# Kernel optimization log

Hardware: AMD Instinct MI355X
Metric: run time of the kernel (lower is better)

Reference implementation:

```python
import jax, jax.numpy as jnp
import numpy as np

B, E, T = 16, 64, 1000
DIM, HEADS, NB_F, LAYERS, NUM_CLASSES = 32, 4, 64, 2, 2
BAND_K = 51
DH = DIM // HEADS  # head dim = 8
EPS = 1e-5


def _layernorm(x, g, b):
    mu = jnp.mean(x, axis=-1, keepdims=True)
    var = jnp.var(x, axis=-1, keepdims=True)
    return (x - mu) * jax.lax.rsqrt(var + EPS) * g + b


def setup_inputs() -> dict:
    key = jax.random.key(0)
    ks = jax.random.split(key, 24)
    d = {}
    d['x'] = jax.random.normal(ks[0], (B, 1, E, T), dtype=jnp.float32)
    # fixed band-pass filters, stacked as one conv: [4 out, 1 in, 1, 51]
    d['band_w'] = jax.random.normal(ks[1], (4, 1, 1, BAND_K), dtype=jnp.float32) * 0.1
    d['pw_w'] = jax.random.normal(ks[2], (DIM, 4), dtype=jnp.float32) * 0.5
    d['bn_g'] = jnp.ones((DIM,), jnp.float32)
    d['bn_b'] = jnp.zeros((DIM,), jnp.float32)
    d['bn_m'] = jnp.zeros((DIM,), jnp.float32)
    d['bn_v'] = jnp.ones((DIM,), jnp.float32)
    s = 1.0 / np.sqrt(DIM)
    L = LAYERS
    d['ln1_g'] = jnp.ones((L, DIM), jnp.float32)
    d['ln1_b'] = jnp.zeros((L, DIM), jnp.float32)
    d['wqkv'] = jax.random.normal(ks[3], (L, DIM, 3 * DIM), jnp.float32) * s
    d['proj_mat'] = jax.random.normal(ks[4], (L, HEADS, DH, NB_F), jnp.float32)
    d['wproj'] = jax.random.normal(ks[5], (L, DIM, DIM), jnp.float32) * s
    d['bproj'] = jnp.zeros((L, DIM), jnp.float32)
    d['ln2_g'] = jnp.ones((L, DIM), jnp.float32)
    d['ln2_b'] = jnp.zeros((L, DIM), jnp.float32)
    d['w1'] = jax.random.normal(ks[6], (L, DIM, 2 * DIM), jnp.float32) * s
    d['b1'] = jnp.zeros((L, 2 * DIM), jnp.float32)
    d['w2'] = jax.random.normal(ks[7], (L, 2 * DIM, DIM), jnp.float32) * (1.0 / np.sqrt(2 * DIM))
    d['b2'] = jnp.zeros((L, DIM), jnp.float32)
    d['norm_g'] = jnp.ones((DIM,), jnp.float32)
    d['norm_b'] = jnp.zeros((DIM,), jnp.float32)
    d['pool_w'] = jax.random.normal(ks[8], (DIM, 1), jnp.float32) * s
    d['pool_b'] = jnp.zeros((1,), jnp.float32)
    d['fc_w'] = jax.random.normal(ks[9], (DIM, NUM_CLASSES), jnp.float32) * s
    d['fc_b'] = jnp.zeros((NUM_CLASSES,), jnp.float32)
    return d


def _favor(x, pm):
    # x: [B,N,C] -> [B,N,H,F] feature map
    b, n, c = x.shape
    xh = x.reshape(b, n, HEADS, DH)
    p = jnp.einsum('bnhd,hdf->bnhf', xh, pm)
    return jax.nn.elu(p) + 1.0


def _attn(x, wqkv, pm, wproj, bproj):
    b, n, c = x.shape
    qkv = x @ wqkv  # [B,N,3C]
    q, k, v = jnp.split(qkv, 3, axis=-1)
    Q = _favor(q, pm)
    K = _favor(k, pm)
    V = v.reshape(b, n, HEADS, DH)
    # NOTE: faithful to source — KV sums over batch AND sequence
    KV = jnp.einsum('bnhf,bnhd->hfd', K, V)
    Z = 1.0 / jnp.einsum('bnhf,hfd->bnh', Q, KV)
    out = jnp.einsum('bnhf,hfd->bnhd', Q, KV) * Z[..., None]
    return out.reshape(b, n, c) @ wproj + bproj


def _tokenize(x, band_w, pw_w, bn_g, bn_b, bn_m, bn_v):
    pad = BAND_K // 2
    xc = jax.lax.conv_general_dilated(
        x, band_w, window_strides=(1, 1), padding=((0, 0), (pad, pad)),
        dimension_numbers=('NCHW', 'OIHW', 'NCHW'))  # [B,4,E,T]
    h = jnp.einsum('bcet,oc->boet', xc, pw_w)  # 1x1 conv -> [B,DIM,E,T]
    h = (h - bn_m[:, None, None]) * jax.lax.rsqrt(bn_v[:, None, None] + EPS) \
        * bn_g[:, None, None] + bn_b[:, None, None]
    h = jax.nn.gelu(h, approximate=False)
    b, c, e, t = h.shape
    h = h.reshape(b, c, e, t // 4, 4).mean(axis=-1)  # AvgPool (1,4)
    h = h.reshape(b, c, e * (t // 4))
    return jnp.transpose(h, (0, 2, 1))  # [B, N, DIM]


def reference(x, band_w, pw_w, bn_g, bn_b, bn_m, bn_v, ln1_g, ln1_b, wqkv,
              proj_mat, wproj, bproj, ln2_g, ln2_b, w1, b1, w2, b2,
              norm_g, norm_b, pool_w, pool_b, fc_w, fc_b):
    h = _tokenize(x, band_w, pw_w, bn_g, bn_b, bn_m, bn_v)
    for l in range(LAYERS):
        h = h + _attn(_layernorm(h, ln1_g[l], ln1_b[l]), wqkv[l], proj_mat[l],
                      wproj[l], bproj[l])
        m = _layernorm(h, ln2_g[l], ln2_b[l])
        m = jax.nn.gelu(m @ w1[l] + b1[l], approximate=False) @ w2[l] + b2[l]
        h = h + m
    h = _layernorm(h, norm_g, norm_b)
    w = jax.nn.softmax(h @ pool_w + pool_b, axis=1)  # [B,N,1]
    pooled = jnp.sum(w * h, axis=1)  # [B,DIM]
    return pooled @ fc_w + fc_b
```

## Files before the change

### kernel.cpp

```cpp
#include <hip/hip_runtime.h>
#include <math.h>

#define NTOK   256000
#define TOKB   16000
#define EPS    1e-5f

__device__ __forceinline__ float gelu_f(float x){
  return 0.5f*x*(1.0f+erff(x*0.70710678118654752440f));
}
__device__ __forceinline__ float elu1_f(float x){
  return x>0.0f ? x+1.0f : __expf(x);
}

__global__ __launch_bounds__(256) void k_tokenize(
    const float* __restrict__ x, const float* __restrict__ band_w,
    const float* __restrict__ pw_w, const float* __restrict__ bn_g,
    const float* __restrict__ bn_b, const float* __restrict__ bn_m,
    const float* __restrict__ bn_v, float* __restrict__ hout)
{
  __shared__ float sx[1050];
  __shared__ float sbw[4][51];
  __shared__ float spw[32][4];
  __shared__ float sscale[32], sshift[32];
  const int tid = threadIdx.x;
  const int b = blockIdx.x >> 6, e = blockIdx.x & 63;
  const float* xr = x + (size_t)(b*64 + e)*1000;
  for (int i=tid;i<1050;i+=256){ int t=i-25; sx[i]=(t>=0&&t<1000)?xr[t]:0.0f; }
  for (int i=tid;i<204;i+=256){ sbw[i/51][i%51] = band_w[i]; }
  for (int i=tid;i<128;i+=256){ spw[i>>2][i&3] = pw_w[i]; }
  if (tid<32){ float sc = bn_g[tid]*rsqrtf(bn_v[tid]+EPS);
               sscale[tid]=sc; sshift[tid]=bn_b[tid]-bn_m[tid]*sc; }
  __syncthreads();
  const int tp = tid;
  if (tp < 250) {
    float acc[32];
    #pragma unroll
    for (int o=0;o<32;o++) acc[o]=0.0f;
    for (int j=0;j<4;j++){
      const int t = 4*tp+j;
      float c0=0,c1=0,c2=0,c3=0;
      for (int k=0;k<51;k++){
        float xv = sx[t+k];
        c0 += xv*sbw[0][k]; c1 += xv*sbw[1][k];
        c2 += xv*sbw[2][k]; c3 += xv*sbw[3][k];
      }
      #pragma unroll
      for (int o=0;o<32;o++){
        float hv = spw[o][0]*c0 + spw[o][1]*c1 + spw[o][2]*c2 + spw[o][3]*c3;
        hv = hv*sscale[o] + sshift[o];
        acc[o] += gelu_f(hv);
      }
    }
    const int tok = b*TOKB + e*250 + tp;
    float4* dst = (float4*)(hout + (size_t)tok*32);
    #pragma unroll
    for (int o8=0;o8<8;o8++)
      dst[o8] = make_float4(acc[o8*4]*0.25f, acc[o8*4+1]*0.25f,
                            acc[o8*4+2]*0.25f, acc[o8*4+3]*0.25f);
  }
}

__global__ __launch_bounds__(256) void k_kv_partial(
    const float* __restrict__ hbuf, const float* __restrict__ ln1_g,
    const float* __restrict__ ln1_b, const float* __restrict__ wqkv,
    const float* __restrict__ proj_mat, float* __restrict__ kvpart, int l)
{
  __shared__ __align__(16) float sk[128][36];
  __shared__ __align__(16) float sv[128][36];
  __shared__ __align__(16) float swkT[64][32];
  __shared__ float sg[32], sb[32];
  const int tid = threadIdx.x;
  const float* W = wqkv + l*32*96;
  for (int idx=tid;idx<2048;idx+=256){
    int i = idx&31, j = idx>>5;
    swkT[j][i] = W[i*96 + 32 + j];
  }
  if (tid<32){ sg[tid]=ln1_g[l*32+tid]; sb[tid]=ln1_b[l*32+tid]; }
  __syncthreads();
  {
    const int tloc = tid>>1, half = tid&1;
    const int tok = blockIdx.x*128 + tloc;
    float hx[32];
    const float4* src = (const float4*)(hbuf + (size_t)tok*32);
    #pragma unroll
    for (int i=0;i<8;i++){ float4 v4=src[i]; hx[4*i]=v4.x; hx[4*i+1]=v4.y; hx[4*i+2]=v4.z; hx[4*i+3]=v4.w; }
    float mu=0;
    #pragma unroll
    for (int i=0;i<32;i++) mu += hx[i];
    mu *= (1.0f/32.0f);
    float vs=0;
    #pragma unroll
    for (int i=0;i<32;i++){ float d=hx[i]-mu; vs += d*d; }
    const float inv = rsqrtf(vs*(1.0f/32.0f)+EPS);
    float xn[32];
    #pragma unroll
    for (int i=0;i<32;i++) xn[i] = (hx[i]-mu)*inv*sg[i]+sb[i];
    const int j0 = half*16;
    #pragma unroll 4
    for (int jj=0;jj<16;jj++){
      const int j = j0+jj;
      const float4* wk4 = (const float4*)&swkT[j][0];
      const float4* wv4 = (const float4*)&swkT[32+j][0];
      float ka=0, va=0;
      #pragma unroll
      for (int i4=0;i4<8;i4++){
        float4 wk = wk4[i4], wv = wv4[i4];
        ka += xn[4*i4+0]*wk.x + xn[4*i4+1]*wk.y + xn[4*i4+2]*wk.z + xn[4*i4+3]*wk.w;
        va += xn[4*i4+0]*wv.x + xn[4*i4+1]*wv.y + xn[4*i4+2]*wv.z + xn[4*i4+3]*wv.w;
      }
      sk[tloc][j]=ka; sv[tloc][j]=va;
    }
  }
  __syncthreads();
  const int hh = tid>>6, f = tid&63;
  float pm0,pm1,pm2,pm3,pm4,pm5,pm6,pm7;
  {
    const float* pmp = proj_mat + ((size_t)(l*4+hh)*8)*64 + f;
    pm0=pmp[0]; pm1=pmp[64]; pm2=pmp[128]; pm3=pmp[192];
    pm4=pmp[256]; pm5=pmp[320]; pm6=pmp[384]; pm7=pmp[448];
  }
  float a0=0,a1=0,a2=0,a3=0,a4=0,a5=0,a6=0,a7=0;
  #pragma unroll 4
  for (int t=0;t<128;t++){
    const float4* k4 = (const float4*)&sk[t][hh*8];
    const float4* v4 = (const float4*)&sv[t][hh*8];
    float4 ka = k4[0], kb = k4[1];
    float kd = ka.x*pm0 + ka.y*pm1 + ka.z*pm2 + ka.w*pm3
             + kb.x*pm4 + kb.y*pm5 + kb.z*pm6 + kb.w*pm7;
    const float Kf = elu1_f(kd);
    float4 va = v4[0], vb = v4[1];
    a0 += Kf*va.x; a1 += Kf*va.y; a2 += Kf*va.z; a3 += Kf*va.w;
    a4 += Kf*vb.x; a5 += Kf*vb.y; a6 += Kf*vb.z; a7 += Kf*vb.w;
  }
  float4* dst = (float4*)(kvpart + (size_t)blockIdx.x*2048 + tid*8);
  dst[0] = make_float4(a0,a1,a2,a3);
  dst[1] = make_float4(a4,a5,a6,a7);
}

__global__ __launch_bounds__(256) void k_kv_reduce1(
    const float* __restrict__ kvpart, float* __restrict__ p2)
{
  const int chunk = blockIdx.x >> 3;
  const int e = (blockIdx.x&7)*256 + threadIdx.x;
  float acc=0.0f;
  const int base = chunk*200;
  for (int ab=0; ab<200; ab++) acc += kvpart[(size_t)(base+ab)*2048 + e];
  p2[chunk*2048 + e] = acc;
}

__global__ __launch_bounds__(256) void k_kv_reduce2(
    const float* __restrict__ p2, float* __restrict__ KV)
{
  const int hf = threadIdx.x;
  float acc[8];
  #pragma unroll
  for (int d=0;d<8;d++) acc[d]=0.0f;
  for (int c=0;c<10;c++){
    #pragma unroll
    for (int d=0;d<8;d++) acc[d] += p2[c*2048 + hf*8 + d];
  }
  #pragma unroll
  for (int d=0;d<8;d++) KV[hf*8+d]=acc[d];
}

__global__ __launch_bounds__(256) void k_attn(
    float* __restrict__ hbuf,
    const float* __restrict__ ln1_g, const float* __restrict__ ln1_b,
    const float* __restrict__ wqkv, const float* __restrict__ proj_mat,
    const float* __restrict__ wproj, const float* __restrict__ bproj,
    const float* __restrict__ KV, int l)
{
  __shared__ __align__(16) float swqT[32][32];
  __shared__ __align__(16) float pmT[4][64][8];
  __shared__ __align__(16) float kvT[4][64][8];
  __shared__ __align__(16) float wpT[32][32];
  __shared__ float s1g[32],s1b[32],sbp[32];
  const int tid = threadIdx.x;
  for (int idx=tid;idx<1024;idx+=256){
    int j=idx>>5, i=idx&31;
    swqT[j][i] = wqkv[l*3072 + i*96 + j];
    wpT[j][i]  = wproj[l*1024 + i*32 + j];
  }
  for (int idx=tid;idx<2048;idx+=256){
    int hh=idx>>9, f=(idx>>3)&63, d=idx&7;
    pmT[hh][f][d] = proj_mat[l*2048 + hh*512 + d*64 + f];
    (&kvT[0][0][0])[idx] = KV[idx];
  }
  if (tid<32){ s1g[tid]=ln1_g[l*32+tid]; s1b[tid]=ln1_b[l*32+tid];
               sbp[tid]=bproj[l*32+tid]; }
  __syncthreads();

  const int tok = blockIdx.x*256 + tid;
  float4* hp = (float4*)(hbuf + (size_t)tok*32);

  float xn[32];
  {
    float hx[32];
    #pragma unroll
    for (int i=0;i<8;i++){ float4 v=hp[i]; hx[4*i]=v.x; hx[4*i+1]=v.y; hx[4*i+2]=v.z; hx[4*i+3]=v.w; }
    float mu=0;
    #pragma unroll
    for (int i=0;i<32;i++) mu += hx[i];
    mu *= (1.0f/32.0f);
    float vs=0;
    #pragma unroll
    for (int i=0;i<32;i++){ float d=hx[i]-mu; vs += d*d; }
    const float inv = rsqrtf(vs*(1.0f/32.0f)+EPS);
    #pragma unroll
    for (int i=0;i<32;i++) xn[i] = (hx[i]-mu)*inv*s1g[i]+s1b[i];
  }

  float att[32];
  #pragma unroll
  for (int hh=0;hh<4;hh++){
    float qh[8];
    #pragma unroll
    for (int d=0;d<8;d++){
      const float4* wr = (const float4*)&swqT[hh*8+d][0];
      float a=0;
      #pragma unroll
      for (int i4=0;i4<8;i4++){
        float4 w = wr[i4];
        a += xn[4*i4+0]*w.x + xn[4*i4+1]*w.y + xn[4*i4+2]*w.z + xn[4*i4+3]*w.w;
      }
      qh[d]=a;
    }
    float ao[8];
    #pragma unroll
    for (int d=0;d<8;d++) ao[d]=0.0f;
    for (int f=0;f<64;f++){
      const float4* pm4 = (const float4*)&pmT[hh][f][0];
      float4 pa = pm4[0], pb = pm4[1];
      float qd = qh[0]*pa.x+qh[1]*pa.y+qh[2]*pa.z+qh[3]*pa.w
               + qh[4]*pb.x+qh[5]*pb.y+qh[6]*pb.z+qh[7]*pb.w;
      const float Qf = elu1_f(qd);
      const float4* kv4 = (const float4*)&kvT[hh][f][0];
      float4 va = kv4[0], vb = kv4[1];
      ao[0] += Qf*va.x; ao[1] += Qf*va.y; ao[2] += Qf*va.z; ao[3] += Qf*va.w;
      ao[4] += Qf*vb.x; ao[5] += Qf*vb.y; ao[6] += Qf*vb.z; ao[7] += Qf*vb.w;
    }
    const float den = ao[0]+ao[1]+ao[2]+ao[3]+ao[4]+ao[5]+ao[6]+ao[7];
    const float z = 1.0f/den;
    #pragma unroll
    for (int d=0;d<8;d++) att[hh*8+d] = ao[d]*z;
  }

  const float4* sbp4 = (const float4*)sbp;
  for (int o4=0;o4<8;o4++){
    float4 bb = sbp4[o4];
    float p0=bb.x, p1=bb.y, p2=bb.z, p3=bb.w;
    const float4* w0 = (const float4*)&wpT[o4*4+0][0];
    const float4* w1r= (const float4*)&wpT[o4*4+1][0];
    const float4* w2r= (const float4*)&wpT[o4*4+2][0];
    const float4* w3 = (const float4*)&wpT[o4*4+3][0];
    #pragma unroll
    for (int i4=0;i4<8;i4++){
      float4 a0=w0[i4], a1=w1r[i4], a2=w2r[i4], a3=w3[i4];
      p0 += att[4*i4+0]*a0.x + att[4*i4+1]*a0.y + att[4*i4+2]*a0.z + att[4*i4+3]*a0.w;
      p1 += att[4*i4+0]*a1.x + att[4*i4+1]*a1.y + att[4*i4+2]*a1.z + att[4*i4+3]*a1.w;
      p2 += att[4*i4+0]*a2.x + att[4*i4+1]*a2.y + att[4*i4+2]*a2.z + att[4*i4+3]*a2.w;
      p3 += att[4*i4+0]*a3.x + att[4*i4+1]*a3.y + att[4*i4+2]*a3.z + att[4*i4+3]*a3.w;
    }
    float4 hx4 = hp[o4];
    hp[o4] = make_float4(hx4.x+p0, hx4.y+p1, hx4.z+p2, hx4.w+p3);
  }
}

__global__ __launch_bounds__(256) void k_ffn(
    float* __restrict__ hbuf,
    const float* __restrict__ ln2_g, const float* __restrict__ ln2_b,
    const float* __restrict__ w1, const float* __restrict__ b1,
    const float* __restrict__ w2, const float* __restrict__ b2, int l)
{
  __shared__ __align__(16) float w1T[64][32];
  __shared__ __align__(16) float sw2[64][32];
  __shared__ float s2g[32],s2b[32],sb1[64],sb2[32];
  const int tid = threadIdx.x;
  for (int idx=tid;idx<2048;idx+=256){
    int j=idx>>5, i=idx&31;
    w1T[j][i] = w1[l*2048 + i*64 + j];
    (&sw2[0][0])[idx] = w2[l*2048 + idx];
  }
  if (tid<32){ s2g[tid]=ln2_g[l*32+tid]; s2b[tid]=ln2_b[l*32+tid];
               sb2[tid]=b2[l*32+tid]; }
  if (tid<64) sb1[tid]=b1[l*64+tid];
  __syncthreads();

  const int tok = blockIdx.x*256 + tid;
  float4* hp = (float4*)(hbuf + (size_t)tok*32);

  float m[32];
  {
    float hx[32];
    #pragma unroll
    for (int i=0;i<8;i++){ float4 v=hp[i]; hx[4*i]=v.x; hx[4*i+1]=v.y; hx[4*i+2]=v.z; hx[4*i+3]=v.w; }
    float mu=0;
    #pragma unroll
    for (int i=0;i<32;i++) mu += hx[i];
    mu *= (1.0f/32.0f);
    float vs=0;
    #pragma unroll
    for (int i=0;i<32;i++){ float d=hx[i]-mu; vs += d*d; }
    const float inv = rsqrtf(vs*(1.0f/32.0f)+EPS);
    #pragma unroll
    for (int i=0;i<32;i++) m[i] = (hx[i]-mu)*inv*s2g[i]+s2b[i];
  }

  float f[32];
  const float4* sb24 = (const float4*)sb2;
  #pragma unroll
  for (int c4=0;c4<8;c4++){
    float4 b = sb24[c4];
    f[4*c4+0]=b.x; f[4*c4+1]=b.y; f[4*c4+2]=b.z; f[4*c4+3]=b.w;
  }

  for (int j=0;j<64;j++){
    const float4* w1r = (const float4*)&w1T[j][0];
    float g = sb1[j];
    #pragma unroll
    for (int i4=0;i4<8;i4++){
      float4 w = w1r[i4];
      g += m[4*i4+0]*w.x + m[4*i4+1]*w.y + m[4*i4+2]*w.z + m[4*i4+3]*w.w;
    }
    const float gg = gelu_f(g);
    const float4* w2r = (const float4*)&sw2[j][0];
    #pragma unroll
    for (int c4=0;c4<8;c4++){
      float4 w = w2r[c4];
      f[4*c4+0] += gg*w.x; f[4*c4+1] += gg*w.y;
      f[4*c4+2] += gg*w.z; f[4*c4+3] += gg*w.w;
    }
  }

  #pragma unroll
  for (int o4=0;o4<8;o4++){
    float4 hx4 = hp[o4];
    hp[o4] = make_float4(hx4.x+f[4*o4+0], hx4.y+f[4*o4+1],
                         hx4.z+f[4*o4+2], hx4.w+f[4*o4+3]);
  }
}

__global__ __launch_bounds__(256) void k_pool_score(
    const float* __restrict__ hbuf, const float* __restrict__ ng,
    const float* __restrict__ nb, const float* __restrict__ pw,
    const float* __restrict__ pb, float* __restrict__ s)
{
  const int tok = blockIdx.x*256 + threadIdx.x;
  float hx[32];
  const float4* src = (const float4*)(hbuf + (size_t)tok*32);
  #pragma unroll
  for (int i=0;i<8;i++){ float4 v4=src[i]; hx[4*i]=v4.x; hx[4*i+1]=v4.y; hx[4*i+2]=v4.z; hx[4*i+3]=v4.w; }
  float mu=0;
  #pragma unroll
  for (int i=0;i<32;i++) mu += hx[i];
  mu *= (1.0f/32.0f);
  float vs=0;
  #pragma unroll
  for (int i=0;i<32;i++){ float d=hx[i]-mu; vs += d*d; }
  const float inv = rsqrtf(vs*(1.0f/32.0f)+EPS);
  float sv = pb[0];
  #pragma unroll
  for (int i=0;i<32;i++) sv += ((hx[i]-mu)*inv*ng[i]+nb[i])*pw[i];
  s[tok]=sv;
}

__global__ __launch_bounds__(256) void k_softmax_stats(
    const float* __restrict__ s, float* __restrict__ bmax, float* __restrict__ bsum)
{
  __shared__ float red[256];
  __shared__ float smax_sh;
  const int b = blockIdx.x, tid = threadIdx.x;
  const float* sbp = s + (size_t)b*TOKB;
  float mx = -INFINITY;
  for (int i=tid;i<TOKB;i+=256) mx = fmaxf(mx, sbp[i]);
  red[tid]=mx; __syncthreads();
  for (int st=128;st>0;st>>=1){ if(tid<st) red[tid]=fmaxf(red[tid],red[tid+st]); __syncthreads(); }
  if (tid==0) smax_sh = red[0];
  __syncthreads();
  const float smax = smax_sh;
  float acc=0.0f;
  for (int i=tid;i<TOKB;i+=256) acc += __expf(sbp[i]-smax);
  __syncthreads();
  red[tid]=acc; __syncthreads();
  for (int st=128;st>0;st>>=1){ if(tid<st) red[tid]+=red[tid+st]; __syncthreads(); }
  if (tid==0){ bmax[b]=smax; bsum[b]=red[0]; }
}

__global__ __launch_bounds__(256) void k_pool_partial(
    const float* __restrict__ hbuf, const float* __restrict__ ng,
    const float* __restrict__ nb, const float* __restrict__ s,
    const float* __restrict__ bmax, float* __restrict__ pp)
{
  __shared__ float red[256][33];
  const int b = blockIdx.x/63, ch = blockIdx.x%63;
  const int tid = threadIdx.x;
  const int n = ch*256+tid;
  if (n < TOKB) {
    const int tok = b*TOKB+n;
    float hx[32];
    const float4* src = (const float4*)(hbuf + (size_t)tok*32);
    #pragma unroll
    for (int i=0;i<8;i++){ float4 v4=src[i]; hx[4*i]=v4.x; hx[4*i+1]=v4.y; hx[4*i+2]=v4.z; hx[4*i+3]=v4.w; }
    float mu=0;
    #pragma unroll
    for (int i=0;i<32;i++) mu += hx[i];
    mu *= (1.0f/32.0f);
    float vs=0;
    #pragma unroll
    for (int i=0;i<32;i++){ float d=hx[i]-mu; vs += d*d; }
    const float inv = rsqrtf(vs*(1.0f/32.0f)+EPS);
    const float w = __expf(s[tok]-bmax[b]);
    #pragma unroll
    for (int i=0;i<32;i++) red[tid][i] = w*((hx[i]-mu)*inv*ng[i]+nb[i]);
  } else {
    #pragma unroll
    for (int i=0;i<32;i++) red[tid][i]=0.0f;
  }
  __syncthreads();
  if (tid<32){
    float acc=0.0f;
    for (int t=0;t<256;t++) acc += red[t][tid];
    pp[(size_t)blockIdx.x*32 + tid] = acc;
  }
}

__global__ __launch_bounds__(64) void k_pool_final(
    const float* __restrict__ pp, const float* __restrict__ bsum,
    const float* __restrict__ fcw, const float* __restrict__ fcb,
    float* __restrict__ out)
{
  __shared__ float sp[32];
  const int b = blockIdx.x, tid = threadIdx.x;
  if (tid<32){
    float acc=0.0f;
    for (int ch=0;ch<63;ch++) acc += pp[(size_t)(b*63+ch)*32+tid];
    sp[tid] = acc / bsum[b];
  }
  __syncthreads();
  if (tid<2){
    float v = fcb[tid];
    for (int o=0;o<32;o++) v += sp[o]*fcw[o*2+tid];
    out[b*2+tid]=v;
  }
}

extern "C" void kernel_launch(void* const* d_in, const int* in_sizes, int n_in,
                              void* d_out, int out_size, void* d_ws, size_t ws_size,
                              hipStream_t stream)
{
  const float* x      = (const float*)d_in[0];
  const float* band_w = (const float*)d_in[1];
  const float* pw_w   = (const float*)d_in[2];
  const float* bn_g   = (const float*)d_in[3];
  const float* bn_b   = (const float*)d_in[4];
  const float* bn_m   = (const float*)d_in[5];
  const float* bn_v   = (const float*)d_in[6];
  const float* ln1_g  = (const float*)d_in[7];
  const float* ln1_b  = (const float*)d_in[8];
  const float* wqkv   = (const float*)d_in[9];
  const float* proj   = (const float*)d_in[10];
  const float* wproj  = (const float*)d_in[11];
  const float* bprojp = (const float*)d_in[12];
  const float* ln2_g  = (const float*)d_in[13];
  const float* ln2_b  = (const float*)d_in[14];
  const float* w1     = (const float*)d_in[15];
  const float* b1     = (const float*)d_in[16];
  const float* w2     = (const float*)d_in[17];
  const float* b2     = (const float*)d_in[18];
  const float* norm_g = (const float*)d_in[19];
  const float* norm_b = (const float*)d_in[20];
  const float* pool_w = (const float*)d_in[21];
  const float* pool_b = (const float*)d_in[22];
  const float* fc_w   = (const float*)d_in[23];
  const float* fc_b   = (const float*)d_in[24];
  float* out = (float*)d_out;
  float* ws  = (float*)d_ws;

  float* hbuf  = ws;
  float* kvp   = hbuf + 8192000;
  float* p2    = kvp  + 4096000;
  float* KV    = p2   + 20480;
  float* sbuf  = KV   + 2048;
  float* bmax  = sbuf + 256000;
  float* bsum  = bmax + 16;
  float* pp    = bsum + 16;

  k_tokenize<<<1024,256,0,stream>>>(x, band_w, pw_w, bn_g, bn_b, bn_m, bn_v, hbuf);
  for (int l=0;l<2;l++){
    k_kv_partial<<<2000,256,0,stream>>>(hbuf, ln1_g, ln1_b, wqkv, proj, kvp, l);
    k_kv_reduce1<<<80,256,0,stream>>>(kvp, p2);
    k_kv_reduce2<<<1,256,0,stream>>>(p2, KV);
    k_attn<<<1000,256,0,stream>>>(hbuf, ln1_g, ln1_b, wqkv, proj, wproj, bprojp, KV, l);
    k_ffn<<<1000,256,0,stream>>>(hbuf, ln2_g, ln2_b, w1, b1, w2, b2, l);
  }
  k_pool_score<<<1000,256,0,stream>>>(hbuf, norm_g, norm_b, pool_w, pool_b, sbuf);
  k_softmax_stats<<<16,256,0,stream>>>(sbuf, bmax, bsum);
  k_pool_partial<<<16*63,256,0,stream>>>(hbuf, norm_g, norm_b, sbuf, bmax, pp);
  k_pool_final<<<16,64,0,stream>>>(pp, bsum, fc_w, fc_b, out);
}
```

Before: 627.9 us.

## Read uniform weights directly from global memory instead of staging in LDS

Removes per-block shared-memory staging of weights (wq, wk/wv, wproj, proj_mat, KV, w1, w2, LN params) in the kv, attention and FFN kernels. Threads read the wave-uniform weights straight from global memory, which the compiler can turn into scalar loads. A new prep kernel pre-transposes proj_mat and w1 once for both layers so these reads are contiguous. The k/v projection is restructured into outer-product accumulation with 16 register accumulators, and the thread-to-token mapping is changed. This drops barriers and LDS traffic in exchange for higher register pressure and reliance on scalar or constant cache behaviour.

Result: slower. 729.3 us (+16.1%).

```diff
diff --git a/kernel.cpp b/kernel.cpp
--- a/kernel.cpp
+++ b/kernel.cpp
@@ -10,6 +10,19 @@
 }
 __device__ __forceinline__ float elu1_f(float x){
   return x>0.0f ? x+1.0f : __expf(x);
+}
+
+__global__ __launch_bounds__(256) void k_prep(
+    const float* __restrict__ proj_mat, const float* __restrict__ w1,
+    float* __restrict__ pmT, float* __restrict__ w1T)
+{
+  const int i = blockIdx.x*256 + threadIdx.x;
+  if (i < 4096){
+    const int l=i>>11, h=(i>>9)&3, f=(i>>3)&63, d=i&7;
+    pmT[i] = proj_mat[l*2048 + h*512 + d*64 + f];
+    const int j=(i>>5)&63, i2=i&31;
+    w1T[i] = w1[l*2048 + i2*64 + j];
+  }
 }
 
 __global__ __launch_bounds__(256) void k_tokenize(
@@ -61,24 +74,16 @@
 }
 
 __global__ __launch_bounds__(256) void k_kv_partial(
-    const float* __restrict__ hbuf, const float* __restrict__ ln1_g,
-    const float* __restrict__ ln1_b, const float* __restrict__ wqkv,
-    const float* __restrict__ proj_mat, float* __restrict__ kvpart, int l)
+    const float* __restrict__ hbuf, const float* __restrict__ lg,
+    const float* __restrict__ lb, const float* __restrict__ W,
+    const float* __restrict__ pm,
+    float* __restrict__ kvpart)
 {
   __shared__ __align__(16) float sk[128][36];
   __shared__ __align__(16) float sv[128][36];
-  __shared__ __align__(16) float swkT[64][32];
-  __shared__ float sg[32], sb[32];
   const int tid = threadIdx.x;
-  const float* W = wqkv + l*32*96;
-  for (int idx=tid;idx<2048;idx+=256){
-    int i = idx&31, j = idx>>5;
-    swkT[j][i] = W[i*96 + 32 + j];
-  }
-  if (tid<32){ sg[tid]=ln1_g[l*32+tid]; sb[tid]=ln1_b[l*32+tid]; }
-  __syncthreads();
   {
-    const int tloc = tid>>1, half = tid&1;
+    const int tloc = tid & 127, half = tid >> 7;
     const int tok = blockIdx.x*128 + tloc;
     float hx[32];
     const float4* src = (const float4*)(hbuf + (size_t)tok*32);
@@ -94,28 +99,31 @@
     const float inv = rsqrtf(vs*(1.0f/32.0f)+EPS);
     float xn[32];
     #pragma unroll
-    for (int i=0;i<32;i++) xn[i] = (hx[i]-mu)*inv*sg[i]+sb[i];
+    for (int i=0;i<32;i++) xn[i] = (hx[i]-mu)*inv*lg[i]+lb[i];
     const int j0 = half*16;
-    #pragma unroll 4
-    for (int jj=0;jj<16;jj++){
-      const int j = j0+jj;
-      const float4* wk4 = (const float4*)&swkT[j][0];
-      const float4* wv4 = (const float4*)&swkT[32+j][0];
-      float ka=0, va=0;
+    float ka[16], va[16];
+    #pragma unroll
+    for (int jj=0;jj<16;jj++){ ka[jj]=0.0f; va[jj]=0.0f; }
+    #pragma unroll
+    for (int i=0;i<32;i++){
+      const float* rk = W + i*96 + 32 + j0;
+      const float* rv = W + i*96 + 64 + j0;
       #pragma unroll
-      for (int i4=0;i4<8;i4++){
-        float4 wk = wk4[i4], wv = wv4[i4];
-        ka += xn[4*i4+0]*wk.x + xn[4*i4+1]*wk.y + xn[4*i4+2]*wk.z + xn[4*i4+3]*wk.w;
-        va += xn[4*i4+0]*wv.x + xn[4*i4+1]*wv.y + xn[4*i4+2]*wv.z + xn[4*i4+3]*wv.w;
-      }
-      sk[tloc][j]=ka; sv[tloc][j]=va;
+      for (int jj=0;jj<16;jj++){ ka[jj] += xn[i]*rk[jj]; va[jj] += xn[i]*rv[jj]; }
+    }
+    float4* skp = (float4*)&sk[tloc][j0];
+    float4* svp = (float4*)&sv[tloc][j0];
+    #pragma unroll
+    for (int q4=0;q4<4;q4++){
+      skp[q4] = make_float4(ka[4*q4],ka[4*q4+1],ka[4*q4+2],ka[4*q4+3]);
+      svp[q4] = make_float4(va[4*q4],va[4*q4+1],va[4*q4+2],va[4*q4+3]);
     }
   }
   __syncthreads();
   const int hh = tid>>6, f = tid&63;
   float pm0,pm1,pm2,pm3,pm4,pm5,pm6,pm7;
   {
-    const float* pmp = proj_mat + ((size_t)(l*4+hh)*8)*64 + f;
+    const float* pmp = pm + (size_t)hh*512 + f;
     pm0=pmp[0]; pm1=pmp[64]; pm2=pmp[128]; pm3=pmp[192];
     pm4=pmp[256]; pm5=pmp[320]; pm6=pmp[384]; pm7=pmp[448];
   }
@@ -165,32 +173,14 @@
 
 __global__ __launch_bounds__(256) void k_attn(
     float* __restrict__ hbuf,
-    const float* __restrict__ ln1_g, const float* __restrict__ ln1_b,
-    const float* __restrict__ wqkv, const float* __restrict__ proj_mat,
-    const float* __restrict__ wproj, const float* __restrict__ bproj,
-    const float* __restrict__ KV, int l)
-{
-  __shared__ __align__(16) float swqT[32][32];
-  __shared__ __align__(16) float pmT[4][64][8];
-  __shared__ __align__(16) float kvT[4][64][8];
-  __shared__ __align__(16) float wpT[32][32];
-  __shared__ float s1g[32],s1b[32],sbp[32];
-  const int tid = threadIdx.x;
-  for (int idx=tid;idx<1024;idx+=256){
-    int j=idx>>5, i=idx&31;
-    swqT[j][i] = wqkv[l*3072 + i*96 + j];
-    wpT[j][i]  = wproj[l*1024 + i*32 + j];
-  }
-  for (int idx=tid;idx<2048;idx+=256){
-    int hh=idx>>9, f=(idx>>3)&63, d=idx&7;
-    pmT[hh][f][d] = proj_mat[l*2048 + hh*512 + d*64 + f];
-    (&kvT[0][0][0])[idx] = KV[idx];
-  }
-  if (tid<32){ s1g[tid]=ln1_g[l*32+tid]; s1b[tid]=ln1_b[l*32+tid];
-               sbp[tid]=bproj[l*32+tid]; }
-  __syncthreads();
-
-  const int tok = blockIdx.x*256 + tid;
+    const float* __restrict__ lg, const float* __restrict__ lb,
+    const float* __restrict__ wq,
+    const float* __restrict__ pmT,
+    const float* __restrict__ wp,
+    const float* __restrict__ bp,
+    const float* __restrict__ KV)
+{
+  const int tok = blockIdx.x*256 + threadIdx.x;
   float4* hp = (float4*)(hbuf + (size_t)tok*32);
 
   float xn[32];
@@ -207,86 +197,66 @@
     for (int i=0;i<32;i++){ float d=hx[i]-mu; vs += d*d; }
     const float inv = rsqrtf(vs*(1.0f/32.0f)+EPS);
     #pragma unroll
-    for (int i=0;i<32;i++) xn[i] = (hx[i]-mu)*inv*s1g[i]+s1b[i];
-  }
-
-  float att[32];
+    for (int i=0;i<32;i++) xn[i] = (hx[i]-mu)*inv*lg[i]+lb[i];
+  }
+
+  float q[32];
+  #pragma unroll
+  for (int j=0;j<32;j++) q[j]=0.0f;
+  #pragma unroll
+  for (int i=0;i<32;i++){
+    const float* r = wq + i*96;
+    #pragma unroll
+    for (int j=0;j<32;j++) q[j] += xn[i]*r[j];
+  }
+
   #pragma unroll
   for (int hh=0;hh<4;hh++){
-    float qh[8];
-    #pragma unroll
-    for (int d=0;d<8;d++){
-      const float4* wr = (const float4*)&swqT[hh*8+d][0];
-      float a=0;
-      #pragma unroll
-      for (int i4=0;i4<8;i4++){
-        float4 w = wr[i4];
-        a += xn[4*i4+0]*w.x + xn[4*i4+1]*w.y + xn[4*i4+2]*w.z + xn[4*i4+3]*w.w;
-      }
-      qh[d]=a;
-    }
     float ao[8];
     #pragma unroll
     for (int d=0;d<8;d++) ao[d]=0.0f;
+    #pragma unroll 4
     for (int f=0;f<64;f++){
-      const float4* pm4 = (const float4*)&pmT[hh][f][0];
-      float4 pa = pm4[0], pb = pm4[1];
-      float qd = qh[0]*pa.x+qh[1]*pa.y+qh[2]*pa.z+qh[3]*pa.w
-               + qh[4]*pb.x+qh[5]*pb.y+qh[6]*pb.z+qh[7]*pb.w;
+      const float* pm8 = pmT + hh*512 + f*8;
+      float qd = q[hh*8+0]*pm8[0] + q[hh*8+1]*pm8[1] + q[hh*8+2]*pm8[2] + q[hh*8+3]*pm8[3]
+               + q[hh*8+4]*pm8[4] + q[hh*8+5]*pm8[5] + q[hh*8+6]*pm8[6] + q[hh*8+7]*pm8[7];
       const float Qf = elu1_f(qd);
-      const float4* kv4 = (const float4*)&kvT[hh][f][0];
-      float4 va = kv4[0], vb = kv4[1];
-      ao[0] += Qf*va.x; ao[1] += Qf*va.y; ao[2] += Qf*va.z; ao[3] += Qf*va.w;
-      ao[4] += Qf*vb.x; ao[5] += Qf*vb.y; ao[6] += Qf*vb.z; ao[7] += Qf*vb.w;
+      const float* kv8 = KV + hh*512 + f*8;
+      ao[0] += Qf*kv8[0]; ao[1] += Qf*kv8[1]; ao[2] += Qf*kv8[2]; ao[3] += Qf*kv8[3];
+      ao[4] += Qf*kv8[4]; ao[5] += Qf*kv8[5]; ao[6] += Qf*kv8[6]; ao[7] += Qf*kv8[7];
     }
     const float den = ao[0]+ao[1]+ao[2]+ao[3]+ao[4]+ao[5]+ao[6]+ao[7];
     const float z = 1.0f/den;
     #pragma unroll
-    for (int d=0;d<8;d++) att[hh*8+d] = ao[d]*z;
-  }
-
-  const float4* sbp4 = (const float4*)sbp;
+    for (int d=0;d<8;d++) q[hh*8+d] = ao[d]*z;
+  }
+
+  float p[32];
+  #pragma unroll
+  for (int o=0;o<32;o++) p[o] = bp[o];
+  #pragma unroll
+  for (int i=0;i<32;i++){
+    const float* r = wp + i*32;
+    #pragma unroll
+    for (int o=0;o<32;o++) p[o] += q[i]*r[o];
+  }
+  #pragma unroll
   for (int o4=0;o4<8;o4++){
-    float4 bb = sbp4[o4];
-    float p0=bb.x, p1=bb.y, p2=bb.z, p3=bb.w;
-    const float4* w0 = (const float4*)&wpT[o4*4+0][0];
-    const float4* w1r= (const float4*)&wpT[o4*4+1][0];
-    const float4* w2r= (const float4*)&wpT[o4*4+2][0];
-    const float4* w3 = (const float4*)&wpT[o4*4+3][0];
-    #pragma unroll
-    for (int i4=0;i4<8;i4++){
-      float4 a0=w0[i4], a1=w1r[i4], a2=w2r[i4], a3=w3[i4];
-      p0 += att[4*i4+0]*a0.x + att[4*i4+1]*a0.y + att[4*i4+2]*a0.z + att[4*i4+3]*a0.w;
-      p1 += att[4*i4+0]*a1.x + att[4*i4+1]*a1.y + att[4*i4+2]*a1.z + att[4*i4+3]*a1.w;
-      p2 += att[4*i4+0]*a2.x + att[4*i4+1]*a2.y + att[4*i4+2]*a2.z + att[4*i4+3]*a2.w;
-      p3 += att[4*i4+0]*a3.x + att[4*i4+1]*a3.y + att[4*i4+2]*a3.z + att[4*i4+3]*a3.w;
-    }
     float4 hx4 = hp[o4];
-    hp[o4] = make_float4(hx4.x+p0, hx4.y+p1, hx4.z+p2, hx4.w+p3);
+    hp[o4] = make_float4(hx4.x+p[4*o4+0], hx4.y+p[4*o4+1],
+                         hx4.z+p[4*o4+2], hx4.w+p[4*o4+3]);
   }
 }
 
 __global__ __launch_bounds__(256) void k_ffn(
     float* __restrict__ hbuf,
-    const float* __restrict__ ln2_g, const float* __restrict__ ln2_b,
-    const float* __restrict__ w1, const float* __restrict__ b1,
-    const float* __restrict__ w2, const float* __restrict__ b2, int l)
-{
-  __shared__ __align__(16) float w1T[64][32];
-  __shared__ __align__(16) float sw2[64][32];
-  __shared__ float s2g[32],s2b[32],sb1[64],sb2[32];
-  const int tid = threadIdx.x;
-  for (int idx=tid;idx<2048;idx+=256){
-    int j=idx>>5, i=idx&31;
-    w1T[j][i] = w1[l*2048 + i*64 + j];
-    (&sw2[0][0])[idx] = w2[l*2048 + idx];
-  }
-  if (tid<32){ s2g[tid]=ln2_g[l*32+tid]; s2b[tid]=ln2_b[l*32+tid];
-               sb2[tid]=b2[l*32+tid]; }
-  if (tid<64) sb1[tid]=b1[l*64+tid];
-  __syncthreads();
-
-  const int tok = blockIdx.x*256 + tid;
+    const float* __restrict__ lg, const float* __restrict__ lb,
+    const float* __restrict__ w1T,
+    const float* __restrict__ b1,
+    const float* __restrict__ w2,
+    const float* __restrict__ b2)
+{
+  const int tok = blockIdx.x*256 + threadIdx.x;
   float4* hp = (float4*)(hbuf + (size_t)tok*32);
 
   float m[32];
@@ -303,33 +273,23 @@
     for (int i=0;i<32;i++){ float d=hx[i]-mu; vs += d*d; }
     const float inv = rsqrtf(vs*(1.0f/32.0f)+EPS);
     #pragma unroll
-    for (int i=0;i<32;i++) m[i] = (hx[i]-mu)*inv*s2g[i]+s2b[i];
+    for (int i=0;i<32;i++) m[i] = (hx[i]-mu)*inv*lg[i]+lb[i];
   }
 
   float f[32];
-  const float4* sb24 = (const float4*)sb2;
-  #pragma unroll
-  for (int c4=0;c4<8;c4++){
-    float4 b = sb24[c4];
-    f[4*c4+0]=b.x; f[4*c4+1]=b.y; f[4*c4+2]=b.z; f[4*c4+3]=b.w;
-  }
-
+  #pragma unroll
+  for (int c=0;c<32;c++) f[c] = b2[c];
+
+  #pragma unroll 4
   for (int j=0;j<64;j++){
-    const float4* w1r = (const float4*)&w1T[j][0];
-    float g = sb1[j];
-    #pragma unroll
-    for (int i4=0;i4<8;i4++){
-      float4 w = w1r[i4];
-      g += m[4*i4+0]*w.x + m[4*i4+1]*w.y + m[4*i4+2]*w.z + m[4*i4+3]*w.w;
-    }
+    const float* r1 = w1T + j*32;
+    float g = b1[j];
+    #pragma unroll
+    for (int i=0;i<32;i++) g += m[i]*r1[i];
     const float gg = gelu_f(g);
-    const float4* w2r = (const float4*)&sw2[j][0];
-    #pragma unroll
-    for (int c4=0;c4<8;c4++){
-      float4 w = w2r[c4];
-      f[4*c4+0] += gg*w.x; f[4*c4+1] += gg*w.y;
-      f[4*c4+2] += gg*w.z; f[4*c4+3] += gg*w.w;
-    }
+    const float* r2 = w2 + j*32;
+    #pragma unroll
+    for (int c=0;c<32;c++) f[c] += gg*r2[c];
   }
 
   #pragma unroll
@@ -480,18 +440,25 @@
   float* kvp   = hbuf + 8192000;
   float* p2    = kvp  + 4096000;
   float* KV    = p2   + 20480;
-  float* sbuf  = KV   + 2048;
+  float* pmT   = KV   + 2048;
+  float* w1T   = pmT  + 4096;
+  float* sbuf  = w1T  + 4096;
   float* bmax  = sbuf + 256000;
   float* bsum  = bmax + 16;
   float* pp    = bsum + 16;
 
+  k_prep<<<16,256,0,stream>>>(proj, w1, pmT, w1T);
   k_tokenize<<<1024,256,0,stream>>>(x, band_w, pw_w, bn_g, bn_b, bn_m, bn_v, hbuf);
   for (int l=0;l<2;l++){
-    k_kv_partial<<<2000,256,0,stream>>>(hbuf, ln1_g, ln1_b, wqkv, proj, kvp, l);
+    k_kv_partial<<<2000,256,0,stream>>>(hbuf, ln1_g+l*32, ln1_b+l*32,
+                                        wqkv+l*3072, proj+l*2048, kvp);
     k_kv_reduce1<<<80,256,0,stream>>>(kvp, p2);
     k_kv_reduce2<<<1,256,0,stream>>>(p2, KV);
-    k_attn<<<1000,256,0,stream>>>(hbuf, ln1_g, ln1_b, wqkv, proj, wproj, bprojp, KV, l);
-    k_ffn<<<1000,256,0,stream>>>(hbuf, ln2_g, ln2_b, w1, b1, w2, b2, l);
+    k_attn<<<1000,256,0,stream>>>(hbuf, ln1_g+l*32, ln1_b+l*32,
+                                  wqkv+l*3072, pmT+l*2048,
+                                  wproj+l*1024, bprojp+l*32, KV);
+    k_ffn<<<1000,256,0,stream>>>(hbuf, ln2_g+l*32, ln2_b+l*32,
+                                 w1T+l*2048, b1+l*64, w2+l*2048, b2+l*32);
   }
   k_pool_score<<<1000,256,0,stream>>>(hbuf, norm_g, norm_b, pool_w, pool_b, sbuf);
   k_softmax_stats<<<16,256,0,stream>>>(sbuf, bmax, bsum);
```
